# Performance work log

Hardware: AMD Instinct MI355X
Metric: run time of the kernel (lower is better)

The kernel has to match this reference:

```python
import jax, jax.numpy as jnp
import numpy as np

L, D, B, N, E, T = 3, 64, 1024, 131072, 1048576, 16
CH, HID = L * D, (L * D) // 2  # channel_dim=192, reduction=2 -> 96
BN_EPS = 1e-5


def setup_inputs() -> dict:
    key = jax.random.key(0)
    ks = jax.random.split(key, 20)
    rn = lambda k, sh, s=0.1: jax.random.normal(k, sh, jnp.float32) * s
    return {
        "query_x": rn(ks[0], (N, D), 1.0),
        "corpus_x": rn(ks[1], (N, D), 1.0),
        "query_edge_index": jax.random.randint(ks[2], (2, E), 0, N),
        "corpus_edge_index": jax.random.randint(ks[3], (2, E), 0, N),
        "query_graph_idx": jnp.sort(jax.random.randint(ks[4], (N,), 0, B)),
        "corpus_graph_idx": jnp.sort(jax.random.randint(ks[5], (N,), 0, B)),
        "gin_w1": rn(ks[6], (L, D, D)),
        "gin_b1": jnp.zeros((L, D), jnp.float32),
        "gin_w2": rn(ks[7], (L, D, D)),
        "gin_b2": jnp.zeros((L, D), jnp.float32),
        "bn_gamma": jnp.ones((L, D), jnp.float32),
        "bn_beta": jnp.zeros((L, D), jnp.float32),
        "gin_eps": jnp.zeros((L,), jnp.float32),
        "inner_w": rn(ks[8], (L, D, D)),
        "inner_b": jnp.zeros((L, D), jnp.float32),
        "outer_w": rn(ks[9], (L, D, D)),
        "outer_b": jnp.zeros((L, D), jnp.float32),
        "conv_w1": rn(ks[10], (CH, HID)),
        "conv_b1": jnp.zeros((HID,), jnp.float32),
        "conv_w2": rn(ks[11], (HID, HID)),
        "conv_b2": jnp.zeros((HID,), jnp.float32),
        "score_w1": rn(ks[12], (HID, 16)),
        "score_b1": jnp.zeros((16,), jnp.float32),
        "score_w2": rn(ks[13], (16, 1)),
        "score_b2": jnp.zeros((1,), jnp.float32),
        "ntn_w": rn(ks[14], (D, D, T), 0.05),
        "ntn_wb": rn(ks[15], (T, 2 * D), 0.05),
        "ntn_bias": jnp.zeros((T,), jnp.float32),
        "sim_w1": rn(ks[16], (T, T)),
        "sim_b1": jnp.zeros((T,), jnp.float32),
        "sim_w2": rn(ks[17], (T, 1)),
        "sim_b2": jnp.zeros((1,), jnp.float32),
        "alpha": jnp.ones((1,), jnp.float32),
        "beta": jnp.ones((1,), jnp.float32),
    }


def _encode(x, edge_index, graph_idx, p):
    """EncodingLayer: per layer GINConv -> ReLU -> inner MLP -> segment-sum pool -> outer MLP."""
    src, dst = edge_index[0], edge_index[1]
    feats = []
    for i in range(L):
        agg = jax.ops.segment_sum(x[src], dst, num_segments=N)  # neighbor sum (gather->scatter)
        h = (1.0 + p["gin_eps"][i]) * x + agg                    # GIN aggregation
        h = jax.nn.relu(h @ p["gin_w1"][i] + p["gin_b1"][i]) @ p["gin_w2"][i] + p["gin_b2"][i]
        mu = h.mean(axis=0)
        var = h.var(axis=0)
        h = (h - mu) * jax.lax.rsqrt(var + BN_EPS) * p["bn_gamma"][i] + p["bn_beta"][i]  # BatchNorm1d (train stats)
        x = jax.nn.relu(h)
        inner = jax.nn.relu(x @ p["inner_w"][i] + p["inner_b"][i])
        pooled = jax.ops.segment_sum(inner, graph_idx, num_segments=B)  # [B, D] graph pooling
        feats.append(jax.nn.relu(pooled @ p["outer_w"][i] + p["outer_b"][i]))
    return jnp.concatenate(feats, axis=1)  # [B, L*D]


def reference(query_x, corpus_x, query_edge_index, corpus_edge_index, query_graph_idx, corpus_graph_idx, gin_w1, gin_b1, gin_w2, gin_b2, bn_gamma, bn_beta, gin_eps, inner_w, inner_b, outer_w, outer_b, conv_w1, conv_b1, conv_w2, conv_b2, score_w1, score_b1, score_w2, score_b2, ntn_w, ntn_wb, ntn_bias, sim_w1, sim_b1, sim_w2, sim_b2, alpha, beta):
    p = {"gin_w1": gin_w1, "gin_b1": gin_b1, "gin_w2": gin_w2, "gin_b2": gin_b2,
         "bn_gamma": bn_gamma, "bn_beta": bn_beta, "gin_eps": gin_eps,
         "inner_w": inner_w, "inner_b": inner_b, "outer_w": outer_w, "outer_b": outer_b}
    qf = _encode(query_x, query_edge_index, query_graph_idx, p)   # [B, CH]
    cf = _encode(corpus_x, corpus_edge_index, corpus_graph_idx, p)
    # diff branch: conv_stack + score_layer
    diff = jnp.exp(-jnp.square(qf - cf))
    h = jax.nn.relu(diff @ conv_w1 + conv_b1)
    h = jnp.tanh(h @ conv_w2 + conv_b2)
    score = jax.nn.sigmoid(jax.nn.relu(h @ score_w1 + score_b1) @ score_w2 + score_b2)[:, 0]
    # NTN interaction branch on last-layer (filters[-1]) graph embeddings
    e1, e2 = qf[:, -D:], cf[:, -D:]
    scoring = jnp.einsum('bf,fgt,bg->bt', e1, ntn_w, e2)
    block = jnp.concatenate([e1, e2], axis=1) @ ntn_wb.T
    sim_rep = jax.nn.relu(scoring + block + ntn_bias)
    sim = jax.nn.sigmoid(jax.nn.relu(sim_rep @ sim_w1 + sim_b1) @ sim_w2 + sim_b2)[:, 0]
    return alpha[0] * score + beta[0] * sim  # [B]
```

## Files before the change

kernel.cpp:

```cpp
#include <hip/hip_runtime.h>
#include <hip/hip_bf16.h>

typedef __hip_bfloat16 bf16;
typedef __attribute__((ext_vector_type(8))) short short8;
typedef __attribute__((ext_vector_type(4))) float floatx4;

#define NN     131072
#define NEDGE  1048576
#define BG     1024
#define LAYERS 3
#define TG     8
#define ZTOTM  (768 + 6*BG*64)

__device__ __forceinline__ short f2bf_s(float f){
    union { float f; unsigned u; } x; x.f = f;
    unsigned r = x.u + 0x7fffu + ((x.u >> 16) & 1u);
    return (short)(r >> 16);
}
__device__ __forceinline__ float bf2f_s(short s){
    union { unsigned u; float f; } x; x.u = ((unsigned)(unsigned short)s) << 16;
    return x.f;
}
__device__ __forceinline__ void acc4(const unsigned short* p,
                                     float& a0, float& a1, float& a2, float& a3){
    ushort4 u = *(const ushort4*)p;
    a0 += bf2f_s((short)u.x); a1 += bf2f_s((short)u.y);
    a2 += bf2f_s((short)u.z); a3 += bf2f_s((short)u.w);
}

__global__ __launch_bounds__(256) void k_wprep(
    const float* __restrict__ gw1, const float* __restrict__ gw2,
    const float* __restrict__ iw,
    short* __restrict__ w1h, short* __restrict__ w1l,
    short* __restrict__ w2h, short* __restrict__ w2l,
    short* __restrict__ wih, short* __restrict__ wil)
{
    int i = blockIdx.x*256 + threadIdx.x;
    if (i >= 3*LAYERS*4096) return;
    int msel = i / (LAYERS*4096);
    int rem  = i % (LAYERS*4096);
    int l = rem >> 12, idx = rem & 4095;
    int n = idx >> 6, k = idx & 63;
    const float* src = (msel==0) ? gw1 : (msel==1) ? gw2 : iw;
    float v = src[l*4096 + k*64 + n];
    short hi = f2bf_s(v);
    short lo = f2bf_s(v - bf2f_s(hi));
    short* dh = (msel==0) ? w1h : (msel==1) ? w2h : wih;
    short* dl = (msel==0) ? w1l : (msel==1) ? w2l : wil;
    dh[rem] = hi;
    dl[rem] = lo;
}

__global__ __launch_bounds__(256) void k_cvtM(const float* __restrict__ qx,
                                              const float* __restrict__ cx,
                                              bf16* __restrict__ xh,
                                              int* __restrict__ cnt,
                                              float* __restrict__ zbuf)
{
    int i = blockIdx.x*256 + threadIdx.x;
    float4 v = (i < NN*16) ? ((const float4*)qx)[i]
                           : ((const float4*)cx)[i - NN*16];
    short4 o;
    o.x = f2bf_s(v.x); o.y = f2bf_s(v.y);
    o.z = f2bf_s(v.z); o.w = f2bf_s(v.w);
    ((short4*)xh)[i] = o;
    if (i < 2*NN)   cnt[i]  = 0;
    if (i < ZTOTM)  zbuf[i] = 0.f;
}

__global__ __launch_bounds__(256) void k_histM(const int* __restrict__ qei,
                                               const int* __restrict__ cei,
                                               int* __restrict__ cnt,
                                               int* __restrict__ rank)
{
    int e = blockIdx.x*256 + threadIdx.x;
    int side = e >> 20;
    int el = e & (NEDGE-1);
    const int* ei = side ? cei : qei;
    rank[e] = atomicAdd(cnt + ei[NEDGE + el] + side*NN, 1);
}

__global__ __launch_bounds__(256) void k_scan1M(const int* __restrict__ cnt,
    int* __restrict__ rowptr, int* __restrict__ bsum)
{
    __shared__ int sd[256];
    int t = threadIdx.x;
    int base = blockIdx.x*1024 + t*4;
    int c0 = cnt[base], c1 = cnt[base+1], c2 = cnt[base+2], c3 = cnt[base+3];
    int tsum = c0 + c1 + c2 + c3;
    sd[t] = tsum;
    __syncthreads();
    for (int off = 1; off < 256; off <<= 1) {
        int v = (t >= off) ? sd[t-off] : 0;
        __syncthreads();
        sd[t] += v;
        __syncthreads();
    }
    int excl = sd[t] - tsum;
    rowptr[base]   = excl;
    rowptr[base+1] = excl + c0;
    rowptr[base+2] = excl + c0 + c1;
    rowptr[base+3] = excl + c0 + c1 + c2;
    if (t == 255) bsum[blockIdx.x] = sd[255];
}

__global__ __launch_bounds__(256) void k_scan2M(const int* __restrict__ bsum,
    int* __restrict__ boff, int* __restrict__ rowptr)
{
    __shared__ int sd[256];
    int t = threadIdx.x;
    int v0 = bsum[t];
    sd[t] = v0;
    __syncthreads();
    for (int off = 1; off < 256; off <<= 1) {
        int v = (t >= off) ? sd[t-off] : 0;
        __syncthreads();
        sd[t] += v;
        __syncthreads();
    }
    boff[t] = sd[t] - v0;
    if (t == 0) rowptr[2*NN] = 2*NEDGE;
}

__global__ __launch_bounds__(256) void k_scan3M(int* __restrict__ rowptr,
    const int* __restrict__ boff)
{
    int i = blockIdx.x*256 + threadIdx.x;
    rowptr[i] += boff[i >> 10];
}

__global__ __launch_bounds__(256) void k_fillM(const int* __restrict__ qei,
    const int* __restrict__ cei,
    const int* __restrict__ rowptr, const int* __restrict__ rank,
    int* __restrict__ col)
{
    int e = blockIdx.x*256 + threadIdx.x;
    int side = e >> 20;
    int el = e & (NEDGE-1);
    const int* ei = side ? cei : qei;
    int s = ei[el] + side*NN;
    int d = ei[NEDGE + el] + side*NN;
    col[rowptr[d] + rank[e]] = s;
}

__global__ __launch_bounds__(256) void k_agg_ginM(
    const bf16* __restrict__ xh,
    const int* __restrict__ rowptr, const int* __restrict__ col,
    const float* __restrict__ epsp,
    const short* __restrict__ w1h, const short* __restrict__ w1l,
    const float* __restrict__ b1,
    const short* __restrict__ w2h, const short* __restrict__ w2l,
    const float* __restrict__ b2,
    unsigned short* __restrict__ bigh, float* __restrict__ stats,
    const short* __restrict__ wihp, const short* __restrict__ wilp,
    const float* __restrict__ bip,
    const int* __restrict__ gidx_q, const int* __restrict__ gidx_c,
    float* __restrict__ pool_q, float* __restrict__ pool_c)
{
    __shared__ __align__(16) char buf[4][9472];
    __shared__ float red[2][4][64];
    int bid = blockIdx.x;
    int side = bid >> 10;
    int tid = threadIdx.x, wv = tid >> 6, lane = tid & 63;
    int q = lane >> 4, m = lane & 15;
    int nb = bid*128 + wv*32;
    short* Sh = (short*)buf[wv];
    short* Sl = Sh + 2304;
    float ep = 1.0f + *epsp;
    const short* xs = (const short*)xh;

    short8 A3[2][2];
    if (wihp) {
        #pragma unroll
        for (int mc=0; mc<2; mc++)
          #pragma unroll
          for (int kc=0; kc<2; kc++)
            A3[mc][kc] = *(const short8*)(xs + (((size_t)(nb + mc*16 + m)) << 6)
                                             + kc*32 + q*8);
    }

    int gv = rowptr[nb + (lane < 33 ? lane : 32)];
    int fo = m * 4;
    const unsigned short* xt = (const unsigned short*)xh;

    for (int i = 0; i < 8; i++) {
        int row = i*4 + q;
        int rs = __shfl(gv, row, 64);
        int re = __shfl(gv, row+1, 64);
        float a0=0.f,a1=0.f,a2=0.f,a3=0.f;
        float e0=0.f,e1=0.f,e2=0.f,e3=0.f;
        float g0=0.f,g1=0.f,g2=0.f,g3=0.f;
        float h0=0.f,h1=0.f,h2=0.f,h3=0.f;
        int r = rs;
        for (; r + 4 <= re; r += 4) {
            int ca = col[r], cb = col[r+1], cc = col[r+2], cd = col[r+3];
            acc4(xt + (((size_t)ca) << 6) + fo, a0,a1,a2,a3);
            acc4(xt + (((size_t)cb) << 6) + fo, e0,e1,e2,e3);
            acc4(xt + (((size_t)cc) << 6) + fo, g0,g1,g2,g3);
            acc4(xt + (((size_t)cd) << 6) + fo, h0,h1,h2,h3);
        }
        for (; r < re; r++)
            acc4(xt + (((size_t)col[r]) << 6) + fo, a0,a1,a2,a3);
        a0 += e0 + g0 + h0;
        a1 += e1 + g1 + h1;
        a2 += e2 + g2 + h2;
        a3 += e3 + g3 + h3;
        ushort4 sv = *(const ushort4*)(xt + (((size_t)(nb+row)) << 6) + fo);
        a0 = fmaf(ep, bf2f_s((short)sv.x), a0);
        a1 = fmaf(ep, bf2f_s((short)sv.y), a1);
        a2 = fmaf(ep, bf2f_s((short)sv.z), a2);
        a3 = fmaf(ep, bf2f_s((short)sv.w), a3);
        short4 hh, ll;
        hh.x = f2bf_s(a0); ll.x = f2bf_s(a0 - bf2f_s(hh.x));
        hh.y = f2bf_s(a1); ll.y = f2bf_s(a1 - bf2f_s(hh.y));
        hh.z = f2bf_s(a2); ll.z = f2bf_s(a2 - bf2f_s(hh.z));
        hh.w = f2bf_s(a3); ll.w = f2bf_s(a3 - bf2f_s(hh.w));
        *(short4*)(Sh + row*72 + fo) = hh;
        *(short4*)(Sl + row*72 + fo) = ll;
    }
    __syncthreads();

    short8 Ah[2][2], Al[2][2];
    #pragma unroll
    for (int mc=0; mc<2; mc++)
      #pragma unroll
      for (int kc=0; kc<2; kc++){
        Ah[mc][kc] = *(const short8*)(Sh + (mc*16+m)*72 + kc*32 + q*8);
        Al[mc][kc] = *(const short8*)(Sl + (mc*16+m)*72 + kc*32 + q*8);
      }
    floatx4 acc[2][4];
    #pragma unroll
    for (int mc=0;mc<2;mc++)
      #pragma unroll
      for (int nc=0;nc<4;nc++) acc[mc][nc] = (floatx4){0.f,0.f,0.f,0.f};
    #pragma unroll
    for (int nc=0;nc<4;nc++){
      #pragma unroll
      for (int kc=0;kc<2;kc++){
        short8 bh = *(const short8*)(w1h + (nc*16+m)*64 + kc*32 + q*8);
        short8 bl = *(const short8*)(w1l + (nc*16+m)*64 + kc*32 + q*8);
        #pragma unroll
        for (int mc=0;mc<2;mc++){
          acc[mc][nc] = __builtin_amdgcn_mfma_f32_16x16x32_bf16(Ah[mc][kc], bh, acc[mc][nc],0,0,0);
          acc[mc][nc] = __builtin_amdgcn_mfma_f32_16x16x32_bf16(Al[mc][kc], bh, acc[mc][nc],0,0,0);
          acc[mc][nc] = __builtin_amdgcn_mfma_f32_16x16x32_bf16(Ah[mc][kc], bl, acc[mc][nc],0,0,0);
        }
      }
    }

    #pragma unroll
    for (int nc=0;nc<4;nc++){
      float bia = b1[nc*16+m];
      #pragma unroll
      for (int mc=0;mc<2;mc++)
        #pragma unroll
        for (int r=0;r<4;r++){
          float v = fmaxf(acc[mc][nc][r] + bia, 0.f);
          int row = mc*16 + q*4 + r, cl = nc*16 + m;
          short hb = f2bf_s(v);
          Sh[row*72+cl] = hb;
          Sl[row*72+cl] = f2bf_s(v - bf2f_s(hb));
        }
    }
    __syncthreads();

    short8 A2h[2][2], A2l[2][2];
    #pragma unroll
    for (int mc=0; mc<2; mc++)
      #pragma unroll
      for (int kc=0; kc<2; kc++){
        A2h[mc][kc] = *(const short8*)(Sh + (mc*16+m)*72 + kc*32 + q*8);
        A2l[mc][kc] = *(const short8*)(Sl + (mc*16+m)*72 + kc*32 + q*8);
      }
    floatx4 acc2[2][4];
    #pragma unroll
    for (int mc=0;mc<2;mc++)
      #pragma unroll
      for (int nc=0;nc<4;nc++) acc2[mc][nc] = (floatx4){0.f,0.f,0.f,0.f};
    #pragma unroll
    for (int nc=0;nc<4;nc++){
      #pragma unroll
      for (int kc=0;kc<2;kc++){
        short8 bh = *(const short8*)(w2h + (nc*16+m)*64 + kc*32 + q*8);
        short8 bl = *(const short8*)(w2l + (nc*16+m)*64 + kc*32 + q*8);
        #pragma unroll
        for (int mc=0;mc<2;mc++){
          acc2[mc][nc] = __builtin_amdgcn_mfma_f32_16x16x32_bf16(A2h[mc][kc], bh, acc2[mc][nc],0,0,0);
          acc2[mc][nc] = __builtin_amdgcn_mfma_f32_16x16x32_bf16(A2l[mc][kc], bh, acc2[mc][nc],0,0,0);
          acc2[mc][nc] = __builtin_amdgcn_mfma_f32_16x16x32_bf16(A2h[mc][kc], bl, acc2[mc][nc],0,0,0);
        }
      }
    }

    #pragma unroll
    for (int nc=0;nc<4;nc++){
      float bia = b2[nc*16+m];
      float s = 0.f, s2 = 0.f;
      #pragma unroll
      for (int mc=0;mc<2;mc++)
        #pragma unroll
        for (int r=0;r<4;r++){
          float v = acc2[mc][nc][r] + bia;
          bigh[(((size_t)(nb + mc*16 + q*4 + r)) << 6) + nc*16 + m] =
              (unsigned short)f2bf_s(v);
          s += v; s2 = fmaf(v, v, s2);
        }
      s  += __shfl_xor(s, 16, 64);  s  += __shfl_xor(s, 32, 64);
      s2 += __shfl_xor(s2,16, 64);  s2 += __shfl_xor(s2,32, 64);
      if (q == 0){ red[0][wv][nc*16+m] = s; red[1][wv][nc*16+m] = s2; }
    }
    __syncthreads();
    if (tid < 128){
      int which = tid >> 6, c = tid & 63;
      float a = red[which][0][c]+red[which][1][c]+red[which][2][c]+red[which][3][c];
      unsafeAtomicAdd(stats + side*128 + which*64 + c, a);
    }

    if (wihp) {
        floatx4 acc3[2][4];
        #pragma unroll
        for (int mc=0;mc<2;mc++)
          #pragma unroll
          for (int nc=0;nc<4;nc++) acc3[mc][nc] = (floatx4){0.f,0.f,0.f,0.f};
        #pragma unroll
        for (int nc=0;nc<4;nc++){
          #pragma unroll
          for (int kc=0;kc<2;kc++){
            short8 bh = *(const short8*)(wihp + (nc*16+m)*64 + kc*32 + q*8);
            short8 bl = *(const short8*)(wilp + (nc*16+m)*64 + kc*32 + q*8);
            #pragma unroll
            for (int mc=0;mc<2;mc++){
              acc3[mc][nc] = __builtin_amdgcn_mfma_f32_16x16x32_bf16(A3[mc][kc], bh, acc3[mc][nc],0,0,0);
              acc3[mc][nc] = __builtin_amdgcn_mfma_f32_16x16x32_bf16(A3[mc][kc], bl, acc3[mc][nc],0,0,0);
            }
          }
        }
        __syncthreads();
        float* P = (float*)buf[wv];
        #pragma unroll
        for (int nc=0;nc<4;nc++){
          float bia = bip[nc*16+m];
          #pragma unroll
          for (int mc=0;mc<2;mc++)
            #pragma unroll
            for (int r=0;r<4;r++){
              float v = fmaxf(acc3[mc][nc][r] + bia, 0.f);
              P[(mc*16 + q*4 + r)*66 + nc*16 + m] = v;
            }
        }
        __syncthreads();

        const int* gidx = side ? gidx_c : gidx_q;
        float* pooled   = side ? pool_c : pool_q;
        int ln = nb - side*NN;
        int gv2 = (lane < 32) ? gidx[ln + lane] : 0;
        int cur = __shfl(gv2, 0, 64);
        float a = 0.f;
        for (int rr = 0; rr < 32; rr++){
            int g = __shfl(gv2, rr, 64);
            if (g != cur){
                unsafeAtomicAdd(pooled + (size_t)cur*64 + lane, a);
                a = 0.f; cur = g;
            }
            a += P[rr*66 + lane];
        }
        unsafeAtomicAdd(pooled + (size_t)cur*64 + lane, a);
    }
}

__global__ __launch_bounds__(256) void k_bn_apply(
    const unsigned short* __restrict__ bigh, const float* __restrict__ stats,
    const float* __restrict__ gam, const float* __restrict__ bet,
    bf16* __restrict__ xh,
    const float* __restrict__ pprev_q, const float* __restrict__ pprev_c,
    const float* __restrict__ owp, const float* __restrict__ obp,
    float* __restrict__ qf, float* __restrict__ cf, int coffp)
{
    __shared__ float scs[128], shs[128];
    int t = threadIdx.x;
    if (t < 128) {
        int side = t >> 6, c = t & 63;
        const float* st = stats + side*128;
        float mu  = st[c]    * (1.0f/NN);
        float ex2 = st[64+c] * (1.0f/NN);
        float var = ex2 - mu*mu;
        float sc  = gam[c] * rsqrtf(var + 1e-5f);
        scs[t] = sc;
        shs[t] = bet[c] - mu*sc;
    }
    if (owp && blockIdx.x < 512) {
        int side = blockIdx.x >> 8;
        int g = (blockIdx.x & 255)*256 + t;
        int bb = g >> 6, j = g & 63;
        const float* pr = (side ? pprev_c : pprev_q) + (size_t)bb*64;
        float a = obp[j];
        for (int k = 0; k < 64; k++) a = fmaf(pr[k], owp[k*64 + j], a);
        (side ? cf : qf)[bb*192 + coffp + j] = fmaxf(a, 0.f);
    }
    __syncthreads();

    int i = blockIdx.x*256 + t;
    ushort4 u = ((const ushort4*)bigh)[i];
    int e = i << 2;
    int base = ((e >> 6) >> 17)*64 + (e & 63);
    short4 o;
    float v0 = fmaxf(fmaf(bf2f_s((short)u.x), scs[base],   shs[base]),   0.f);
    float v1 = fmaxf(fmaf(bf2f_s((short)u.y), scs[base+1], shs[base+1]), 0.f);
    float v2 = fmaxf(fmaf(bf2f_s((short)u.z), scs[base+2], shs[base+2]), 0.f);
    float v3 = fmaxf(fmaf(bf2f_s((short)u.w), scs[base+3], shs[base+3]), 0.f);
    o.x = f2bf_s(v0); o.y = f2bf_s(v1); o.z = f2bf_s(v2); o.w = f2bf_s(v3);
    ((short4*)xh)[i] = o;
}

__global__ __launch_bounds__(256) void k_bn_innerM(
    const unsigned short* __restrict__ bigh, const float* __restrict__ stats,
    const float* __restrict__ gam, const float* __restrict__ bet,
    const short* __restrict__ wih, const short* __restrict__ wil,
    const float* __restrict__ bi,
    bf16* __restrict__ xh,
    const int* __restrict__ gidx_q, const int* __restrict__ gidx_c,
    float* __restrict__ pooled_q, float* __restrict__ pooled_c,
    const float* __restrict__ pprev_q, const float* __restrict__ pprev_c,
    const float* __restrict__ owp, const float* __restrict__ obp,
    float* __restrict__ qf, float* __restrict__ cf, int coffp)
{
    __shared__ __align__(16) char buf[4][9472];
    int bid = blockIdx.x;
    int side = bid >> 10;
    int lb = bid & 1023;
    int tid = threadIdx.x, wv = tid >> 6, lane = tid & 63;
    int q = lane >> 4, m = lane & 15;
    int nb = bid*128 + wv*32;
    short* Sh = (short*)buf[wv];
    short* Sl = Sh + 2304;

    if (owp && lb < 256) {
        int g = lb*256 + tid;
        int bb = g >> 6, j = g & 63;
        const float* pr = (side ? pprev_c : pprev_q) + (size_t)bb*64;
        float a = obp[j];
        for (int k = 0; k < 64; k++) a = fmaf(pr[k], owp[k*64 + j], a);
        (side ? cf : qf)[bb*192 + coffp + j] = fmaxf(a, 0.f);
    }

    const float* st = stats + side*128;
    float mu  = st[lane]    * (1.0f/NN);
    float ex2 = st[64+lane] * (1.0f/NN);
    float var = ex2 - mu*mu;
    float sc  = gam[lane] * rsqrtf(var + 1e-5f);
    float sh  = bet[lane] - mu*sc;

    for (int rr = 0; rr < 32; rr++){
        float v = bf2f_s((short)bigh[(((size_t)(nb+rr)) << 6) + lane]);
        v = fmaxf(fmaf(v, sc, sh), 0.f);
        xh[(((size_t)(nb+rr)) << 6) + lane] = __float2bfloat16(v);
        short hb = f2bf_s(v);
        Sh[rr*72 + lane] = hb;
        Sl[rr*72 + lane] = f2bf_s(v - bf2f_s(hb));
    }
    __syncthreads();

    short8 A2h[2][2], A2l[2][2];
    #pragma unroll
    for (int mc=0; mc<2; mc++)
      #pragma unroll
      for (int kc=0; kc<2; kc++){
        A2h[mc][kc] = *(const short8*)(Sh + (mc*16+m)*72 + kc*32 + q*8);
        A2l[mc][kc] = *(const short8*)(Sl + (mc*16+m)*72 + kc*32 + q*8);
      }
    floatx4 acc[2][4];
    #pragma unroll
    for (int mc=0;mc<2;mc++)
      #pragma unroll
      for (int nc=0;nc<4;nc++) acc[mc][nc] = (floatx4){0.f,0.f,0.f,0.f};
    #pragma unroll
    for (int nc=0;nc<4;nc++){
      #pragma unroll
      for (int kc=0;kc<2;kc++){
        short8 bh = *(const short8*)(wih + (nc*16+m)*64 + kc*32 + q*8);
        short8 bl = *(const short8*)(wil + (nc*16+m)*64 + kc*32 + q*8);
        #pragma unroll
        for (int mc=0;mc<2;mc++){
          acc[mc][nc] = __builtin_amdgcn_mfma_f32_16x16x32_bf16(A2h[mc][kc], bh, acc[mc][nc],0,0,0);
          acc[mc][nc] = __builtin_amdgcn_mfma_f32_16x16x32_bf16(A2l[mc][kc], bh, acc[mc][nc],0,0,0);
          acc[mc][nc] = __builtin_amdgcn_mfma_f32_16x16x32_bf16(A2h[mc][kc], bl, acc[mc][nc],0,0,0);
        }
      }
    }
    __syncthreads();

    float* P = (float*)buf[wv];
    #pragma unroll
    for (int nc=0;nc<4;nc++){
      float bia = bi[nc*16+m];
      #pragma unroll
      for (int mc=0;mc<2;mc++)
        #pragma unroll
        for (int r=0;r<4;r++){
          float v = fmaxf(acc[mc][nc][r] + bia, 0.f);
          P[(mc*16 + q*4 + r)*66 + nc*16 + m] = v;
        }
    }
    __syncthreads();

    const int* gidx = side ? gidx_c : gidx_q;
    float* pooled   = side ? pooled_c : pooled_q;
    int ln = nb - side*NN;
    int gv = (lane < 32) ? gidx[ln + lane] : 0;
    int cur = __shfl(gv, 0, 64);
    float a = 0.f;
    for (int rr = 0; rr < 32; rr++){
        int g = __shfl(gv, rr, 64);
        if (g != cur){
            unsafeAtomicAdd(pooled + (size_t)cur*64 + lane, a);
            a = 0.f; cur = g;
        }
        a += P[rr*66 + lane];
    }
    unsafeAtomicAdd(pooled + (size_t)cur*64 + lane, a);
}

__global__ __launch_bounds__(256) void k_tailM(
    const float* __restrict__ qf, const float* __restrict__ cf,
    const float* __restrict__ pooled_q2, const float* __restrict__ pooled_c2,
    const float* __restrict__ ow2, const float* __restrict__ ob2,
    const float* __restrict__ cw1, const float* __restrict__ cb1,
    const float* __restrict__ cw2, const float* __restrict__ cb2,
    const float* __restrict__ sw1, const float* __restrict__ sb1,
    const float* __restrict__ sw2, const float* __restrict__ sb2,
    const float* __restrict__ nw,  const float* __restrict__ nwb,
    const float* __restrict__ nb,
    const float* __restrict__ mw1, const float* __restrict__ mb1,
    const float* __restrict__ mw2, const float* __restrict__ mb2,
    const float* __restrict__ alpha, const float* __restrict__ beta,
    float* __restrict__ out)
{
    __shared__ float cws[192*96];
    __shared__ float diff[TG][192];
    __shared__ float e1s[TG][64], e2s[TG][64];
    __shared__ float h1s[TG][96], h2s[TG][96];
    __shared__ float s1s[TG][16], s2s[TG][16], srep[TG][16];
    __shared__ float red[16][16][TG];

    int t = threadIdx.x;
    int b0 = blockIdx.x * TG;

    {
        int b = t >> 5, o = (t & 31) * 2;
        const float* prq = pooled_q2 + (size_t)(b0 + b)*64;
        const float* prc = pooled_c2 + (size_t)(b0 + b)*64;
        float q0 = ob2[o], q1 = ob2[o+1];
        float c0 = ob2[o], c1 = ob2[o+1];
        for (int k = 0; k < 64; k++) {
            float w0 = ow2[k*64 + o], w1 = ow2[k*64 + o + 1];
            float pq = prq[k], pc = prc[k];
            q0 = fmaf(pq, w0, q0); q1 = fmaf(pq, w1, q1);
            c0 = fmaf(pc, w0, c0); c1 = fmaf(pc, w1, c1);
        }
        e1s[b][o]   = fmaxf(q0, 0.f);
        e1s[b][o+1] = fmaxf(q1, 0.f);
        e2s[b][o]   = fmaxf(c0, 0.f);
        e2s[b][o+1] = fmaxf(c1, 0.f);
    }
    for (int i = t; i < 192*96; i += 256) cws[i] = cw1[i];
    __syncthreads();

    for (int i = t; i < TG*192; i += 256) {
        int b = i / 192, f = i % 192;
        float qv = (f < 128) ? qf[(b0+b)*192 + f] : e1s[b][f-128];
        float cv = (f < 128) ? cf[(b0+b)*192 + f] : e2s[b][f-128];
        float d = qv - cv;
        diff[b][f] = __expf(-d*d);
    }
    __syncthreads();

    {
        int b = t >> 5, o = (t & 31) * 3;
        float a0 = cb1[o], a1 = cb1[o+1], a2 = cb1[o+2];
        for (int f = 0; f < 192; f++) {
            float d = diff[b][f];
            const float* w = cws + f*96 + o;
            a0 = fmaf(d, w[0], a0);
            a1 = fmaf(d, w[1], a1);
            a2 = fmaf(d, w[2], a2);
        }
        h1s[b][o] = fmaxf(a0, 0.f);
        h1s[b][o+1] = fmaxf(a1, 0.f);
        h1s[b][o+2] = fmaxf(a2, 0.f);
    }
    __syncthreads();
    for (int i = t; i < 96*96; i += 256) cws[i] = cw2[i];
    __syncthreads();
    {
        int b = t >> 5, o = (t & 31) * 3;
        float a0 = cb2[o], a1 = cb2[o+1], a2 = cb2[o+2];
        for (int f = 0; f < 96; f++) {
            float d = h1s[b][f];
            const float* w = cws + f*96 + o;
            a0 = fmaf(d, w[0], a0);
            a1 = fmaf(d, w[1], a1);
            a2 = fmaf(d, w[2], a2);
        }
        h2s[b][o] = tanhf(a0);
        h2s[b][o+1] = tanhf(a1);
        h2s[b][o+2] = tanhf(a2);
    }
    __syncthreads();
    if (t < TG*16) {
        int b = t >> 4, o = t & 15;
        float a = sb1[o];
        for (int f = 0; f < 96; f++) a = fmaf(h2s[b][f], sw1[f*16+o], a);
        s1s[b][o] = fmaxf(a, 0.f);
    }

    {
        int tt = t & 15, gq = t >> 4;
        int g0 = gq * 4;
        int lane = t & 63;
        float e1v[TG];
        #pragma unroll
        for (int b = 0; b < TG; b++) e1v[b] = e1s[b][lane];
        float v0[TG], v1[TG], v2[TG], v3[TG];
        #pragma unroll
        for (int b = 0; b < TG; b++) { v0[b]=0.f; v1[b]=0.f; v2[b]=0.f; v3[b]=0.f; }
        for (int f = 0; f < 64; f++) {
            const float* wp = nw + ((size_t)f*64 + g0)*16 + tt;
            float w0 = wp[0], w1 = wp[16], w2 = wp[32], w3 = wp[48];
            #pragma unroll
            for (int b = 0; b < TG; b++) {
                float e = __shfl(e1v[b], f, 64);
                v0[b] = fmaf(e, w0, v0[b]);
                v1[b] = fmaf(e, w1, v1[b]);
                v2[b] = fmaf(e, w2, v2[b]);
                v3[b] = fmaf(e, w3, v3[b]);
            }
        }
        #pragma unroll
        for (int b = 0; b < TG; b++) {
            float p = v0[b]*e2s[b][g0] + v1[b]*e2s[b][g0+1]
                    + v2[b]*e2s[b][g0+2] + v3[b]*e2s[b][g0+3];
            red[gq][tt][b] = p;
        }
    }
    __syncthreads();
    if (t < TG*16) {
        int b = t >> 4, tt = t & 15;
        float scv = 0.f;
        #pragma unroll
        for (int gq = 0; gq < 16; gq++) scv += red[gq][tt][b];
        float blk = nb[tt];
        for (int f = 0; f < 64; f++) blk = fmaf(e1s[b][f], nwb[tt*128 + f], blk);
        for (int f = 0; f < 64; f++) blk = fmaf(e2s[b][f], nwb[tt*128 + 64 + f], blk);
        srep[b][tt] = fmaxf(scv + blk, 0.f);
    }
    __syncthreads();
    if (t < TG*16) {
        int b = t >> 4, o = t & 15;
        float a = mb1[o];
        #pragma unroll
        for (int f = 0; f < 16; f++) a = fmaf(srep[b][f], mw1[f*16+o], a);
        s2s[b][o] = fmaxf(a, 0.f);
    }
    __syncthreads();
    if (t < TG) {
        float sco = sb2[0], sm = mb2[0];
        #pragma unroll
        for (int f = 0; f < 16; f++) {
            sco = fmaf(s1s[t][f], sw2[f], sco);
            sm  = fmaf(s2s[t][f], mw2[f], sm);
        }
        float score = 1.f / (1.f + __expf(-sco));
        float sim   = 1.f / (1.f + __expf(-sm));
        out[b0 + t] = alpha[0]*score + beta[0]*sim;
    }
}

extern "C" void kernel_launch(void* const* d_in, const int* in_sizes, int n_in,
                              void* d_out, int out_size, void* d_ws, size_t ws_size,
                              hipStream_t stream)
{
    const float* qx  = (const float*)d_in[0];
    const float* cx  = (const float*)d_in[1];
    const int*   qei = (const int*)d_in[2];
    const int*   cei = (const int*)d_in[3];
    const int*   qgi = (const int*)d_in[4];
    const int*   cgi = (const int*)d_in[5];
    const float* Wgw1 = (const float*)d_in[6];
    const float* Wgb1 = (const float*)d_in[7];
    const float* Wgw2 = (const float*)d_in[8];
    const float* Wgb2 = (const float*)d_in[9];
    const float* Wgam = (const float*)d_in[10];
    const float* Wbet = (const float*)d_in[11];
    const float* Weps = (const float*)d_in[12];
    const float* Wiw  = (const float*)d_in[13];
    const float* Wib  = (const float*)d_in[14];
    const float* Wow  = (const float*)d_in[15];
    const float* Wob  = (const float*)d_in[16];
    const float* Wcw1 = (const float*)d_in[17];
    const float* Wcb1 = (const float*)d_in[18];
    const float* Wcw2 = (const float*)d_in[19];
    const float* Wcb2 = (const float*)d_in[20];
    const float* Wsw1 = (const float*)d_in[21];
    const float* Wsb1 = (const float*)d_in[22];
    const float* Wsw2 = (const float*)d_in[23];
    const float* Wsb2 = (const float*)d_in[24];
    const float* Wnw  = (const float*)d_in[25];
    const float* Wnwb = (const float*)d_in[26];
    const float* Wnb  = (const float*)d_in[27];
    const float* Wmw1 = (const float*)d_in[28];
    const float* Wmb1 = (const float*)d_in[29];
    const float* Wmw2 = (const float*)d_in[30];
    const float* Wmb2 = (const float*)d_in[31];
    const float* Wal  = (const float*)d_in[32];
    const float* Wbe  = (const float*)d_in[33];

    float* F = (float*)d_ws;
    unsigned short* bigh = (unsigned short*)F;
    int*   rank   = (int*)F;
    bf16*  xh     = (bf16*)(F + 8388608);
    float* zbuf   = F + 16777216;
    float* stats3 = zbuf;
    float* pooled3= zbuf + 768;
    float* qf     = F + 16777216 + ZTOTM;
    float* cf     = qf + 196608;
    int*   rowptr = (int*)(cf + 196608);
    int*   cnt    = rowptr + (2*NN + 1);
    int*   col    = cnt + 2*NN;
    int*   bsum   = col + 2*NEDGE;
    int*   boff   = bsum + 256;
    uintptr_t wtb = (uintptr_t)(boff + 256);
    wtb = (wtb + 63) & ~((uintptr_t)63);
    short* w1h = (short*)wtb;
    short* w1l = w1h + 3*4096;
    short* w2h = w1l + 3*4096;
    short* w2l = w2h + 3*4096;
    short* wih = w2l + 3*4096;
    short* wil = wih + 3*4096;

    k_wprep<<<144, 256, 0, stream>>>(Wgw1, Wgw2, Wiw, w1h, w1l, w2h, w2l, wih, wil);
    k_cvtM  <<<16384, 256, 0, stream>>>(qx, cx, xh, cnt, zbuf);
    k_histM <<<8192, 256, 0, stream>>>(qei, cei, cnt, rank);
    k_scan1M<<<256, 256, 0, stream>>>(cnt, rowptr, bsum);
    k_scan2M<<<1, 256, 0, stream>>>(bsum, boff, rowptr);
    k_scan3M<<<1024, 256, 0, stream>>>(rowptr, boff);
    k_fillM <<<8192, 256, 0, stream>>>(qei, cei, rowptr, rank, col);

    float* pq0 = pooled3;
    float* pc0 = pooled3 + (size_t)3*BG*64;
    float* pq1 = pooled3 + (size_t)1*BG*64;
    float* pc1 = pooled3 + (size_t)4*BG*64;
    float* pq2 = pooled3 + (size_t)2*BG*64;
    float* pc2 = pooled3 + (size_t)5*BG*64;

    k_agg_ginM<<<2048, 256, 0, stream>>>(xh, rowptr, col, Weps + 0,
                                         w1h, w1l, Wgb1, w2h, w2l, Wgb2,
                                         bigh, stats3 + 0,
                                         nullptr, nullptr, nullptr,
                                         qgi, cgi, nullptr, nullptr);
    k_bn_apply<<<16384, 256, 0, stream>>>(bigh, stats3 + 0, Wgam, Wbet, xh,
                                          nullptr, nullptr, nullptr, nullptr,
                                          qf, cf, 0);
    k_agg_ginM<<<2048, 256, 0, stream>>>(xh, rowptr, col, Weps + 1,
                                         w1h + 4096, w1l + 4096, Wgb1 + 64,
                                         w2h + 4096, w2l + 4096, Wgb2 + 64,
                                         bigh, stats3 + 256,
                                         wih, wil, Wib,
                                         qgi, cgi, pq0, pc0);
    k_bn_apply<<<16384, 256, 0, stream>>>(bigh, stats3 + 256, Wgam + 64, Wbet + 64, xh,
                                          pq0, pc0, Wow, Wob,
                                          qf, cf, 0);
    k_agg_ginM<<<2048, 256, 0, stream>>>(xh, rowptr, col, Weps + 2,
                                         w1h + 2*4096, w1l + 2*4096, Wgb1 + 128,
                                         w2h + 2*4096, w2l + 2*4096, Wgb2 + 128,
                                         bigh, stats3 + 512,
                                         wih + 4096, wil + 4096, Wib + 64,
                                         qgi, cgi, pq1, pc1);
    k_bn_innerM<<<2048, 256, 0, stream>>>(bigh, stats3 + 512,
                                          Wgam + 128, Wbet + 128,
                                          wih + 2*4096, wil + 2*4096, Wib + 128,
                                          xh, qgi, cgi, pq2, pc2,
                                          pq1, pc1, Wow + 4096, Wob + 64,
                                          qf, cf, 64);

    k_tailM<<<BG/TG, 256, 0, stream>>>(qf, cf, pq2, pc2,
                                       Wow + 2*4096, Wob + 2*64,
                                       Wcw1, Wcb1, Wcw2, Wcb2,
                                       Wsw1, Wsb1, Wsw2, Wsb2,
                                       Wnw, Wnwb, Wnb, Wmw1, Wmb1, Wmw2, Wmb2,
                                       Wal, Wbe, (float*)d_out);
}
```

Measured before the change: 820.5 us.

## Sort CSR neighbor lists by source-node slice to improve gather locality

The CSR build now counts edges per (destination, source slice) pair, with 8 slices of 32K source nodes each. A new kernel turns those counts into per-slice offsets, so each destination's neighbor list comes out grouped by source range. The aim is more locality in the feature gathers of the aggregation kernels, which run three times. The cost is an 8x larger count array to zero and scan, plus one extra kernel launch.

```diff
diff --git a/kernel.cpp b/kernel.cpp
--- a/kernel.cpp
+++ b/kernel.cpp
@@ -10,6 +10,7 @@
 #define BG     1024
 #define LAYERS 3
 #define TG     8
+#define NS     8
 #define ZTOTM  (768 + 6*BG*64)
 
 __device__ __forceinline__ short f2bf_s(float f){
@@ -54,7 +55,7 @@
 __global__ __launch_bounds__(256) void k_cvtM(const float* __restrict__ qx,
                                               const float* __restrict__ cx,
                                               bf16* __restrict__ xh,
-                                              int* __restrict__ cnt,
+                                              int* __restrict__ cnt2,
                                               float* __restrict__ zbuf)
 {
     int i = blockIdx.x*256 + threadIdx.x;
@@ -64,29 +65,39 @@
     o.x = f2bf_s(v.x); o.y = f2bf_s(v.y);
     o.z = f2bf_s(v.z); o.w = f2bf_s(v.w);
     ((short4*)xh)[i] = o;
-    if (i < 2*NN)   cnt[i]  = 0;
-    if (i < ZTOTM)  zbuf[i] = 0.f;
+    if (i < 2*NN*NS) cnt2[i] = 0;
+    if (i < ZTOTM)   zbuf[i] = 0.f;
 }
 
 __global__ __launch_bounds__(256) void k_histM(const int* __restrict__ qei,
                                                const int* __restrict__ cei,
-                                               int* __restrict__ cnt,
+                                               int* __restrict__ cnt2,
                                                int* __restrict__ rank)
 {
     int e = blockIdx.x*256 + threadIdx.x;
     int side = e >> 20;
     int el = e & (NEDGE-1);
     const int* ei = side ? cei : qei;
-    rank[e] = atomicAdd(cnt + ei[NEDGE + el] + side*NN, 1);
-}
-
-__global__ __launch_bounds__(256) void k_scan1M(const int* __restrict__ cnt,
+    int sg = ei[el] + side*NN;
+    int dg = ei[NEDGE + el] + side*NN;
+    int s  = sg >> 15;
+    rank[e] = atomicAdd(cnt2 + dg*NS + s, 1);
+}
+
+__global__ __launch_bounds__(256) void k_scan1M(const int* __restrict__ cnt2,
     int* __restrict__ rowptr, int* __restrict__ bsum)
 {
     __shared__ int sd[256];
     int t = threadIdx.x;
     int base = blockIdx.x*1024 + t*4;
-    int c0 = cnt[base], c1 = cnt[base+1], c2 = cnt[base+2], c3 = cnt[base+3];
+    int c0=0, c1=0, c2=0, c3=0;
+    #pragma unroll
+    for (int s = 0; s < NS; s++){
+        c0 += cnt2[(base+0)*NS + s];
+        c1 += cnt2[(base+1)*NS + s];
+        c2 += cnt2[(base+2)*NS + s];
+        c3 += cnt2[(base+3)*NS + s];
+    }
     int tsum = c0 + c1 + c2 + c3;
     sd[t] = tsum;
     __syncthreads();
@@ -129,18 +140,32 @@
     rowptr[i] += boff[i >> 10];
 }
 
+__global__ __launch_bounds__(256) void k_sliceoffM(int* __restrict__ cnt2,
+    const int* __restrict__ rowptr)
+{
+    int row = blockIdx.x*256 + threadIdx.x;
+    int base = rowptr[row];
+    #pragma unroll
+    for (int s = 0; s < NS; s++){
+        int c = cnt2[row*NS + s];
+        cnt2[row*NS + s] = base;
+        base += c;
+    }
+}
+
 __global__ __launch_bounds__(256) void k_fillM(const int* __restrict__ qei,
     const int* __restrict__ cei,
-    const int* __restrict__ rowptr, const int* __restrict__ rank,
+    const int* __restrict__ cnt2, const int* __restrict__ rank,
     int* __restrict__ col)
 {
     int e = blockIdx.x*256 + threadIdx.x;
     int side = e >> 20;
     int el = e & (NEDGE-1);
     const int* ei = side ? cei : qei;
-    int s = ei[el] + side*NN;
-    int d = ei[NEDGE + el] + side*NN;
-    col[rowptr[d] + rank[e]] = s;
+    int sg = ei[el] + side*NN;
+    int dg = ei[NEDGE + el] + side*NN;
+    int s  = sg >> 15;
+    col[cnt2[dg*NS + s] + rank[e]] = sg;
 }
 
 __global__ __launch_bounds__(256) void k_agg_ginM(
@@ -717,6 +742,7 @@
     float* F = (float*)d_ws;
     unsigned short* bigh = (unsigned short*)F;
     int*   rank   = (int*)F;
+    int*   cnt2   = (int*)F + 2*NEDGE;
     bf16*  xh     = (bf16*)(F + 8388608);
     float* zbuf   = F + 16777216;
     float* stats3 = zbuf;
@@ -724,8 +750,8 @@
     float* qf     = F + 16777216 + ZTOTM;
     float* cf     = qf + 196608;
     int*   rowptr = (int*)(cf + 196608);
-    int*   cnt    = rowptr + (2*NN + 1);
-    int*   col    = cnt + 2*NN;
+    int*   cntold = rowptr + (2*NN + 1);
+    int*   col    = cntold + 2*NN;
     int*   bsum   = col + 2*NEDGE;
     int*   boff   = bsum + 256;
     uintptr_t wtb = (uintptr_t)(boff + 256);
@@ -738,12 +764,13 @@
     short* wil = wih + 3*4096;
 
     k_wprep<<<144, 256, 0, stream>>>(Wgw1, Wgw2, Wiw, w1h, w1l, w2h, w2l, wih, wil);
-    k_cvtM  <<<16384, 256, 0, stream>>>(qx, cx, xh, cnt, zbuf);
-    k_histM <<<8192, 256, 0, stream>>>(qei, cei, cnt, rank);
-    k_scan1M<<<256, 256, 0, stream>>>(cnt, rowptr, bsum);
+    k_cvtM  <<<16384, 256, 0, stream>>>(qx, cx, xh, cnt2, zbuf);
+    k_histM <<<8192, 256, 0, stream>>>(qei, cei, cnt2, rank);
+    k_scan1M<<<256, 256, 0, stream>>>(cnt2, rowptr, bsum);
     k_scan2M<<<1, 256, 0, stream>>>(bsum, boff, rowptr);
     k_scan3M<<<1024, 256, 0, stream>>>(rowptr, boff);
-    k_fillM <<<8192, 256, 0, stream>>>(qei, cei, rowptr, rank, col);
+    k_sliceoffM<<<1024, 256, 0, stream>>>(cnt2, rowptr);
+    k_fillM <<<8192, 256, 0, stream>>>(qei, cei, cnt2, rank, col);
 
     float* pq0 = pooled3;
     float* pc0 = pooled3 + (size_t)3*BG*64;
```

After: 828.7 us. Within noise of the previous version (+1.0%).
